# Optimization experiments

Measured on AMD Instinct MI355X. Metric: run time of the kernel, lower is better.

## Reference

```python
import jax, jax.numpy as jnp
import numpy as np

NUM_NEG_INDICES_FOR_LOSS = 5
NUM_NEG_PAIRS = 64
C, H, W = 256, 512, 512


def setup_inputs() -> dict:
    key = jax.random.key(0)
    k1, k2, k3 = jax.random.split(key, 3)
    feats1 = jax.random.normal(k1, (1, C, H, W), dtype=jnp.float32)
    feats2 = jax.random.normal(k2, (1, C, H, W), dtype=jnp.float32)
    positive_pairs = jax.random.randint(k3, (1, NUM_NEG_PAIRS, 2), 0, H * W, dtype=jnp.int64)
    return {"feats1": feats1, "feats2": feats2, "positive_pairs": positive_pairs}


def reference(feats1, feats2, positive_pairs):
    # feats*: [1, C, H, W]; positive_pairs: [1, P, 2] with P == NUM_NEG_PAIRS
    b, c, h, w = feats1.shape
    f1 = feats1.reshape(c, -1)  # [C, HW] (valid because b == 1, matching torch view)
    f2 = feats2.reshape(c, -1)  # [C, HW]
    idx = positive_pairs[0, :, 0]  # [P] anchor pixel indices into flattened image 1
    sel = f1[:, idx].T             # [P, C] anchor descriptors
    # Squared L2 distance from each anchor to every pixel of image 2 via the
    # ||a||^2 + ||b||^2 - 2 a.b expansion (one [P,C]x[C,HW] GEMM).
    d = (jnp.sum(sel * sel, axis=1, keepdims=True)
         + jnp.sum(f2 * f2, axis=0)[None, :]
         - 2.0 * (sel @ f2))       # [P, HW]
    d = jax.nn.relu(d)             # matches functional.relu (also clamps fp error)
    # Hardest negatives = smallest distances. NOTE: the torch neighborhood-mask
    # exclusion compares a float distance VALUE against an int index array, so
    # it is dead code in practice -> effective math is plain top-k smallest.
    neg_vals, _ = jax.lax.top_k(-d, NUM_NEG_INDICES_FOR_LOSS)  # [P, 5]
    per_pair = jnp.mean(-neg_vals, axis=1)                     # [P]
    return jnp.sum(per_pair) / NUM_NEG_PAIRS
```

## Files before the change

kernel.cpp:

```cpp
#include <hip/hip_runtime.h>
#include <hip/hip_bf16.h>

#define HW_   262144
#define C_    256
#define NP_   64
#define NBLK_ 1024
#define SENT  3.0e38f
#define FIXSCALE 1048576.0

typedef __attribute__((ext_vector_type(8))) __bf16 bf16x8;
typedef __attribute__((ext_vector_type(4))) float f32x4;

__device__ __forceinline__ void top5_insert(float (&t)[5], float v) {
  if (v < t[4]) {
    t[4] = v;
    if (t[4] < t[3]) { float x = t[3]; t[3] = t[4]; t[4] = x; }
    if (t[3] < t[2]) { float x = t[2]; t[2] = t[3]; t[3] = x; }
    if (t[2] < t[1]) { float x = t[1]; t[1] = t[2]; t[2] = x; }
    if (t[1] < t[0]) { float x = t[0]; t[0] = t[1]; t[1] = x; }
  }
}

__global__ void gather_sel_kernel(const float* __restrict__ f1,
                                  const void* __restrict__ pairs,
                                  unsigned short* __restrict__ selb,
                                  float* __restrict__ n_p,
                                  unsigned long long* __restrict__ acc,
                                  unsigned* __restrict__ cnt) {
  __shared__ float red[256];
  __shared__ int sidx;
  const int p = blockIdx.x, t = threadIdx.x;
  if (p == 0 && t == 0) { *acc = 0ull; *cnt = 0u; }
  if (t == 0) {
    const long long* ll = (const long long*)pairs;
    const int* ii = (const int*)pairs;
    bool is64 = true;
    for (int k = 0; k < 8; ++k) {
      long long v = ll[k];
      if (v < 0 || v >= (long long)HW_) is64 = false;
    }
    sidx = is64 ? (int)ll[2 * p] : ii[2 * p];
  }
  __syncthreads();
  const int idx = sidx;
  float v = f1[(size_t)t * HW_ + idx];
  __bf16 b = (__bf16)v;
  selb[p * 256 + t] = __builtin_bit_cast(unsigned short, b);
  red[t] = v * v;
  __syncthreads();
  for (int s = 128; s > 0; s >>= 1) {
    if (t < s) red[t] += red[t + s];
    __syncthreads();
  }
  if (t == 0) n_p[p] = red[0];
}

__global__ __launch_bounds__(512, 4) void dist_topk_kernel(
    const float* __restrict__ f2, const unsigned short* __restrict__ selb,
    const float* __restrict__ n_p, float* __restrict__ cand) {
  __shared__ float smem[64 * 256];
  char* smemB = (char*)smem;
  const int tid = threadIdx.x;
  const int w = tid >> 6, lane = tid & 63;
  const int m_l = lane & 15, kq = lane >> 4;
  const int j0 = blockIdx.x * 256;

  {
    const uint4* src = (const uint4*)selb;
#pragma unroll
    for (int i = 0; i < 4; ++i) {
      const int idx = i * 512 + tid;
      const int m = idx >> 5;
      unsigned off = (unsigned)(idx * 16) ^ ((m & 7) << 4);
      *(uint4*)(smemB + off) = src[idx];
    }
  }
  __syncthreads();

  const unsigned colbase = (unsigned)(j0 + w * 32 + m_l);
  const unsigned rowbase = (unsigned)(kq * 8) * HW_;

  f32x4 acc[4][2];
#pragma unroll
  for (int mt = 0; mt < 4; ++mt)
#pragma unroll
    for (int nt = 0; nt < 2; ++nt) acc[mt][nt] = (f32x4){0.f, 0.f, 0.f, 0.f};
  float njp[2] = {0.f, 0.f};

  float b0[16], b1[16], b2[16];
#define LOADB(BUF, T)                                                          \
  _Pragma("unroll") for (int nt = 0; nt < 2; ++nt)                             \
  _Pragma("unroll") for (int e = 0; e < 8; ++e)                                \
      BUF[nt * 8 + e] =                                                        \
          f2[rowbase + colbase + (unsigned)(((T) * 32 + e) * HW_ + nt * 16)];

  LOADB(b0, 0)
  LOADB(b1, 1)

#define STEP(CUR, NXT, T, PF)                                                   \
  {                                                                             \
    if (PF) { LOADB(NXT, (T) + 2) }                                             \
    bf16x8 afr[4];                                                              \
    _Pragma("unroll") for (int mt = 0; mt < 4; ++mt) {                          \
      unsigned offA =                                                           \
          (unsigned)((mt * 16 + m_l) * 512 + kq * 16 + (T) * 64) ^              \
          ((m_l & 7) << 4);                                                     \
      afr[mt] = *(const bf16x8*)(smemB + offA);                                 \
    }                                                                           \
    bf16x8 bfr[2];                                                              \
    _Pragma("unroll") for (int nt = 0; nt < 2; ++nt) {                          \
      _Pragma("unroll") for (int e = 0; e < 8; ++e) {                           \
        float v = CUR[nt * 8 + e];                                              \
        njp[nt] = fmaf(v, v, njp[nt]);                                          \
        bfr[nt][e] = (__bf16)v;                                                 \
      }                                                                         \
    }                                                                           \
    _Pragma("unroll") for (int mt = 0; mt < 4; ++mt)                            \
      _Pragma("unroll") for (int nt = 0; nt < 2; ++nt)                          \
        acc[mt][nt] = __builtin_amdgcn_mfma_f32_16x16x32_bf16(                  \
            afr[mt], bfr[nt], acc[mt][nt], 0, 0, 0);                            \
  }

  STEP(b0, b2, 0, 1) STEP(b1, b0, 1, 1) STEP(b2, b1, 2, 1) STEP(b0, b2, 3, 1)
  STEP(b1, b0, 4, 1) STEP(b2, b1, 5, 1) STEP(b0, b2, 6, 0) STEP(b1, b0, 7, 0)
#undef STEP
#undef LOADB

  float njc[2];
#pragma unroll
  for (int nt = 0; nt < 2; ++nt) {
    float v = njp[nt];
    v += __shfl_xor(v, 16);
    v += __shfl_xor(v, 32);
    njc[nt] = v;
  }

  __syncthreads();

#pragma unroll
  for (int mt = 0; mt < 4; ++mt) {
#pragma unroll
    for (int r = 0; r < 4; ++r) {
      const int pair = mt * 16 + kq * 4 + r;
      const float np = n_p[pair];
#pragma unroll
      for (int nt = 0; nt < 2; ++nt) {
        const int col = w * 32 + nt * 16 + m_l;
        float d = np + njc[nt] - 2.0f * acc[mt][nt][r];
        smem[pair * 256 + (col ^ (pair & 31))] = fmaxf(d, 0.0f);
      }
    }
  }
  __syncthreads();

  const int pp = tid & 63, q = tid >> 6;
  float t5[5] = {SENT, SENT, SENT, SENT, SENT};
#pragma unroll 4
  for (int i = 0; i < 32; ++i) {
    const int col = q * 32 + i;
    float v = smem[pp * 256 + (col ^ (pp & 31))];
    top5_insert(t5, v);
  }
  __syncthreads();
#pragma unroll
  for (int k = 0; k < 5; ++k) smem[tid * 5 + k] = t5[k];
  __syncthreads();
  if (tid < 64) {
    float m5[5] = {SENT, SENT, SENT, SENT, SENT};
    for (int g = 0; g < 8; ++g)
#pragma unroll
      for (int k = 0; k < 5; ++k) top5_insert(m5, smem[(g * 64 + tid) * 5 + k]);
    float* cc = cand + (size_t)blockIdx.x * (NP_ * 5) + tid * 5;
#pragma unroll
    for (int k = 0; k < 5; ++k) cc[k] = m5[k];
  }
}

__global__ void topk_reduce_kernel(const float* __restrict__ cand,
                                   unsigned long long* __restrict__ acc,
                                   unsigned* __restrict__ cnt,
                                   float* __restrict__ out) {
  __shared__ float lds[256 * 5];
  const int p = blockIdx.x, tid = threadIdx.x;
  float t5[5] = {SENT, SENT, SENT, SENT, SENT};
  for (int b = tid; b < NBLK_; b += 256) {
    const float* cc = cand + (size_t)b * (NP_ * 5) + p * 5;
#pragma unroll
    for (int k = 0; k < 5; ++k) top5_insert(t5, cc[k]);
  }
#pragma unroll
  for (int k = 0; k < 5; ++k) lds[tid * 5 + k] = t5[k];
  __syncthreads();
  float m2[5] = {SENT, SENT, SENT, SENT, SENT};
  if (tid < 32) {
    for (int t2 = tid * 8; t2 < tid * 8 + 8; ++t2)
#pragma unroll
      for (int k = 0; k < 5; ++k) top5_insert(m2, lds[t2 * 5 + k]);
  }
  __syncthreads();
  if (tid < 32) {
#pragma unroll
    for (int k = 0; k < 5; ++k) lds[tid * 5 + k] = m2[k];
  }
  __syncthreads();
  if (tid == 0) {
    float f[5] = {SENT, SENT, SENT, SENT, SENT};
    for (int t2 = 0; t2 < 32; ++t2)
#pragma unroll
      for (int k = 0; k < 5; ++k) top5_insert(f, lds[t2 * 5 + k]);
    const float mean5 = (f[0] + f[1] + f[2] + f[3] + f[4]) * 0.2f;
    const unsigned long long fx =
        (unsigned long long)(long long)(mean5 * FIXSCALE);
    atomicAdd(acc, fx);
    __threadfence();
    const unsigned prev = atomicAdd(cnt, 1u);
    if (prev == NP_ - 1) {
      const unsigned long long total = atomicAdd(acc, 0ull);
      out[0] = (float)((double)total / (FIXSCALE * (double)NP_));
    }
  }
}

extern "C" void kernel_launch(void* const* d_in, const int* in_sizes, int n_in,
                              void* d_out, int out_size, void* d_ws, size_t ws_size,
                              hipStream_t stream) {
  const float* f1 = (const float*)d_in[0];
  const float* f2 = (const float*)d_in[1];
  const void* pairs = d_in[2];
  float* out = (float*)d_out;
  float* ws = (float*)d_ws;

  float*              n_p  = ws;
  unsigned short*     selb = (unsigned short*)(ws + 64);
  float*              cand = ws + 64 + 8192;
  unsigned long long* acc  = (unsigned long long*)(ws + 64 + 8192 + 327680);
  unsigned*           cnt  = (unsigned*)(ws + 64 + 8192 + 327680 + 2);

  gather_sel_kernel<<<NP_, 256, 0, stream>>>(f1, pairs, selb, n_p, acc, cnt);
  dist_topk_kernel<<<NBLK_, 512, 0, stream>>>(f2, selb, n_p, cand);
  topk_reduce_kernel<<<NP_, 256, 0, stream>>>(cand, acc, cnt, out);
}
```

Measured before the change: 82.53 us.

## Warp-specialize distance kernel: producer waves stage bf16 tiles in LDS for MFMA waves

Splits each 256-thread block into two producer waves and two consumer waves. The producers load f2 with coalesced float2 reads, convert to bf16 and write into a double-buffered LDS tile. The consumers run MFMA on that tile, with barriers between stages. Block width is halved to 128 columns, so the grid doubles and the candidate buffer grows. Column norms are now computed from bf16-rounded values, and only half the waves do math, which may reduce MFMA throughput and add barrier overhead.

```diff
diff --git a/kernel.cpp b/kernel.cpp
--- a/kernel.cpp
+++ b/kernel.cpp
@@ -4,7 +4,8 @@
 #define HW_   262144
 #define C_    256
 #define NP_   64
-#define NBLK_ 1024
+#define BCOLS 128
+#define NBLK_ 2048
 #define SENT  3.0e38f
 #define FIXSCALE 1048576.0
 
@@ -55,21 +56,22 @@
   if (t == 0) n_p[p] = red[0];
 }
 
-__global__ __launch_bounds__(512, 4) void dist_topk_kernel(
+__global__ __launch_bounds__(256, 3) void dist_topk_kernel(
     const float* __restrict__ f2, const unsigned short* __restrict__ selb,
     const float* __restrict__ n_p, float* __restrict__ cand) {
-  __shared__ float smem[64 * 256];
-  char* smemB = (char*)smem;
+  __shared__ __align__(16) char smemB[49152];
+  float* smemF = (float*)smemB;
   const int tid = threadIdx.x;
   const int w = tid >> 6, lane = tid & 63;
   const int m_l = lane & 15, kq = lane >> 4;
-  const int j0 = blockIdx.x * 256;
+  const int j0 = blockIdx.x * BCOLS;
+  const int pw = w - 2;
 
   {
     const uint4* src = (const uint4*)selb;
 #pragma unroll
-    for (int i = 0; i < 4; ++i) {
-      const int idx = i * 512 + tid;
+    for (int i = 0; i < 8; ++i) {
+      const int idx = i * 256 + tid;
       const int m = idx >> 5;
       unsigned off = (unsigned)(idx * 16) ^ ((m & 7) << 4);
       *(uint4*)(smemB + off) = src[idx];
@@ -77,29 +79,37 @@
   }
   __syncthreads();
 
-  const unsigned colbase = (unsigned)(j0 + w * 32 + m_l);
-  const unsigned rowbase = (unsigned)(kq * 8) * HW_;
-
-  f32x4 acc[4][2];
-#pragma unroll
-  for (int mt = 0; mt < 4; ++mt)
-#pragma unroll
-    for (int nt = 0; nt < 2; ++nt) acc[mt][nt] = (f32x4){0.f, 0.f, 0.f, 0.f};
-  float njp[2] = {0.f, 0.f};
-
-  float b0[16], b1[16], b2[16];
-#define LOADB(BUF, T)                                                          \
-  _Pragma("unroll") for (int nt = 0; nt < 2; ++nt)                             \
-  _Pragma("unroll") for (int e = 0; e < 8; ++e)                                \
-      BUF[nt * 8 + e] =                                                        \
-          f2[rowbase + colbase + (unsigned)(((T) * 32 + e) * HW_ + nt * 16)];
-
-  LOADB(b0, 0)
-  LOADB(b1, 1)
-
-#define STEP(CUR, NXT, T, PF)                                                   \
+  f32x4 acc[4][4];
+  float njp[4];
+  float2 rP[16];
+  if (w < 2) {
+#pragma unroll
+    for (int mt = 0; mt < 4; ++mt)
+#pragma unroll
+      for (int nt = 0; nt < 4; ++nt) acc[mt][nt] = (f32x4){0.f, 0.f, 0.f, 0.f};
+#pragma unroll
+    for (int nt = 0; nt < 4; ++nt) njp[nt] = 0.f;
+  }
+
+  const float* gbase = f2 + j0 + (lane << 1);
+
+#define LOADP(T)                                                               \
+  _Pragma("unroll") for (int i = 0; i < 16; ++i)                               \
+      rP[i] = *(const float2*)(gbase + (size_t)((T) * 32 + pw * 16 + i) * HW_);
+
+#define WRITEP(BUF)                                                            \
+  _Pragma("unroll") for (int i = 0; i < 16; ++i) {                             \
+    const int r_ = pw * 16 + i;                                                \
+    ushort2 pk;                                                                \
+    pk.x = __builtin_bit_cast(unsigned short, (__bf16)rP[i].x);                \
+    pk.y = __builtin_bit_cast(unsigned short, (__bf16)rP[i].y);                \
+    *(ushort2*)(smemB + 32768 + (BUF) * 8192 + r_ * 256 +                      \
+                (((unsigned)(lane << 2)) ^ (((r_ >> 3) & 3) << 5))) = pk;      \
+  }
+
+#define STEPC(T, BUF)                                                           \
   {                                                                             \
-    if (PF) { LOADB(NXT, (T) + 2) }                                             \
+    const char* Bb = smemB + 32768 + (BUF) * 8192;                              \
     bf16x8 afr[4];                                                              \
     _Pragma("unroll") for (int mt = 0; mt < 4; ++mt) {                          \
       unsigned offA =                                                           \
@@ -107,47 +117,77 @@
           ((m_l & 7) << 4);                                                     \
       afr[mt] = *(const bf16x8*)(smemB + offA);                                 \
     }                                                                           \
-    bf16x8 bfr[2];                                                              \
-    _Pragma("unroll") for (int nt = 0; nt < 2; ++nt) {                          \
+    bf16x8 bfr[4];                                                              \
+    _Pragma("unroll") for (int nt = 0; nt < 4; ++nt) {                          \
+      const unsigned cx =                                                       \
+          ((unsigned)((w * 64 + nt * 16 + m_l) * 2)) ^ ((unsigned)kq << 5);     \
       _Pragma("unroll") for (int e = 0; e < 8; ++e) {                           \
-        float v = CUR[nt * 8 + e];                                              \
-        njp[nt] = fmaf(v, v, njp[nt]);                                          \
-        bfr[nt][e] = (__bf16)v;                                                 \
+        unsigned short us =                                                     \
+            *(const unsigned short*)(Bb + (kq * 8 + e) * 256 + cx);             \
+        bfr[nt][e] = __builtin_bit_cast(__bf16, us);                            \
+        float fv = __builtin_bit_cast(float, (unsigned)us << 16);               \
+        njp[nt] = fmaf(fv, fv, njp[nt]);                                        \
       }                                                                         \
     }                                                                           \
     _Pragma("unroll") for (int mt = 0; mt < 4; ++mt)                            \
-      _Pragma("unroll") for (int nt = 0; nt < 2; ++nt)                          \
+      _Pragma("unroll") for (int nt = 0; nt < 4; ++nt)                          \
         acc[mt][nt] = __builtin_amdgcn_mfma_f32_16x16x32_bf16(                  \
             afr[mt], bfr[nt], acc[mt][nt], 0, 0, 0);                            \
   }
 
-  STEP(b0, b2, 0, 1) STEP(b1, b0, 1, 1) STEP(b2, b1, 2, 1) STEP(b0, b2, 3, 1)
-  STEP(b1, b0, 4, 1) STEP(b2, b1, 5, 1) STEP(b0, b2, 6, 0) STEP(b1, b0, 7, 0)
-#undef STEP
-#undef LOADB
-
-  float njc[2];
-#pragma unroll
-  for (int nt = 0; nt < 2; ++nt) {
-    float v = njp[nt];
-    v += __shfl_xor(v, 16);
-    v += __shfl_xor(v, 32);
-    njc[nt] = v;
-  }
-
-  __syncthreads();
-
-#pragma unroll
-  for (int mt = 0; mt < 4; ++mt) {
-#pragma unroll
-    for (int r = 0; r < 4; ++r) {
-      const int pair = mt * 16 + kq * 4 + r;
-      const float np = n_p[pair];
-#pragma unroll
-      for (int nt = 0; nt < 2; ++nt) {
-        const int col = w * 32 + nt * 16 + m_l;
-        float d = np + njc[nt] - 2.0f * acc[mt][nt][r];
-        smem[pair * 256 + (col ^ (pair & 31))] = fmaxf(d, 0.0f);
+  if (w >= 2) {
+    LOADP(0)
+    WRITEP(0)
+    LOADP(1)
+    asm volatile("s_waitcnt lgkmcnt(0)" ::: "memory");
+  }
+  __builtin_amdgcn_s_barrier();
+  __builtin_amdgcn_sched_barrier(0);
+
+#define ITER(T, LAST)                                                          \
+  if (w < 2) { STEPC(T, (T) & 1) }                                             \
+  else {                                                                       \
+    if ((T) < 7) { WRITEP(((T) + 1) & 1) }                                     \
+    if ((T) < 6) { LOADP((T) + 2) }                                            \
+    asm volatile("s_waitcnt lgkmcnt(0)" ::: "memory");                         \
+  }                                                                            \
+  if (!(LAST)) {                                                               \
+    __builtin_amdgcn_s_barrier();                                              \
+    __builtin_amdgcn_sched_barrier(0);                                         \
+  }
+
+  ITER(0, 0) ITER(1, 0) ITER(2, 0) ITER(3, 0)
+  ITER(4, 0) ITER(5, 0) ITER(6, 0) ITER(7, 1)
+#undef ITER
+#undef STEPC
+#undef WRITEP
+#undef LOADP
+
+  float njc[4];
+  if (w < 2) {
+#pragma unroll
+    for (int nt = 0; nt < 4; ++nt) {
+      float v = njp[nt];
+      v += __shfl_xor(v, 16);
+      v += __shfl_xor(v, 32);
+      njc[nt] = v;
+    }
+  }
+  __syncthreads();
+
+  if (w < 2) {
+#pragma unroll
+    for (int mt = 0; mt < 4; ++mt) {
+#pragma unroll
+      for (int r = 0; r < 4; ++r) {
+        const int pair = mt * 16 + kq * 4 + r;
+        const float np = n_p[pair];
+#pragma unroll
+        for (int nt = 0; nt < 4; ++nt) {
+          const int col = w * 64 + nt * 16 + m_l;
+          float d = np + njc[nt] - 2.0f * acc[mt][nt][r];
+          smemF[pair * 128 + (col ^ (pair & 31))] = fmaxf(d, 0.0f);
+        }
       }
     }
   }
@@ -158,18 +198,18 @@
 #pragma unroll 4
   for (int i = 0; i < 32; ++i) {
     const int col = q * 32 + i;
-    float v = smem[pp * 256 + (col ^ (pp & 31))];
+    float v = smemF[pp * 128 + (col ^ (pp & 31))];
     top5_insert(t5, v);
   }
   __syncthreads();
 #pragma unroll
-  for (int k = 0; k < 5; ++k) smem[tid * 5 + k] = t5[k];
+  for (int k = 0; k < 5; ++k) smemF[tid * 5 + k] = t5[k];
   __syncthreads();
   if (tid < 64) {
     float m5[5] = {SENT, SENT, SENT, SENT, SENT};
-    for (int g = 0; g < 8; ++g)
-#pragma unroll
-      for (int k = 0; k < 5; ++k) top5_insert(m5, smem[(g * 64 + tid) * 5 + k]);
+    for (int g = 0; g < 4; ++g)
+#pragma unroll
+      for (int k = 0; k < 5; ++k) top5_insert(m5, smemF[(g * 64 + tid) * 5 + k]);
     float* cc = cand + (size_t)blockIdx.x * (NP_ * 5) + tid * 5;
 #pragma unroll
     for (int k = 0; k < 5; ++k) cc[k] = m5[k];
@@ -233,10 +273,10 @@
   float*              n_p  = ws;
   unsigned short*     selb = (unsigned short*)(ws + 64);
   float*              cand = ws + 64 + 8192;
-  unsigned long long* acc  = (unsigned long long*)(ws + 64 + 8192 + 327680);
-  unsigned*           cnt  = (unsigned*)(ws + 64 + 8192 + 327680 + 2);
+  unsigned long long* acc  = (unsigned long long*)(ws + 64 + 8192 + 655360);
+  unsigned*           cnt  = (unsigned*)(ws + 64 + 8192 + 655360 + 2);
 
   gather_sel_kernel<<<NP_, 256, 0, stream>>>(f1, pairs, selb, n_p, acc, cnt);
-  dist_topk_kernel<<<NBLK_, 512, 0, stream>>>(f2, selb, n_p, cand);
+  dist_topk_kernel<<<NBLK_, 256, 0, stream>>>(f2, selb, n_p, cand);
   topk_reduce_kernel<<<NP_, 256, 0, stream>>>(cand, acc, cnt, out);
 }
```

After: 100.4 us. +21.6%, slower.
